# Performance work log

Hardware: AMD Instinct MI355X
Metric: run time of the kernel (lower is better)

Reference implementation:

```python
import jax, jax.numpy as jnp
import numpy as np

# Config matching init_kwargs
C, H_IMG, W_IMG = 3, 224, 224
N_PATCHES = 14
PS = H_IMG // N_PATCHES            # 16
INPUT_D = C * PS * PS              # 768
HID = 768
N_HEADS = 12
DH = HID // N_HEADS                # 64
N_BLOCKS = 12
MLP_RATIO = 4
SEQ = N_PATCHES * N_PATCHES + 1    # 197
EPS = 1e-5


def _pos_embed():
    # sin on even dims, cos on odd dims, exponent uses (j - j%2)/d  (faithful to loop)
    i = jnp.arange(SEQ, dtype=jnp.float32)[:, None]
    j = jnp.arange(HID, dtype=jnp.float32)[None, :]
    expo = (j - jnp.mod(j, 2.0)) / HID
    ang = i / jnp.power(10000.0, expo)
    return jnp.where(jnp.mod(jnp.arange(HID), 2) == 0, jnp.sin(ang), jnp.cos(ang))


def setup_inputs() -> dict:
    key = jax.random.key(0)
    ks = jax.random.split(key, 16)
    s = 0.02
    d_ff = MLP_RATIO * HID
    inp = {
        'images': jax.random.normal(ks[0], (16, C, H_IMG, W_IMG), dtype=jnp.float32),
        'w_map': jax.random.normal(ks[1], (HID, INPUT_D), dtype=jnp.float32) * s,
        'b_map': jnp.zeros((HID,), dtype=jnp.float32),
        'class_token': jax.random.uniform(ks[2], (1, HID), dtype=jnp.float32),
        'pos_embed': _pos_embed(),
        'qw': jax.random.normal(ks[3], (N_BLOCKS, N_HEADS, DH, DH), dtype=jnp.float32) * s,
        'qb': jnp.zeros((N_BLOCKS, N_HEADS, DH), dtype=jnp.float32),
        'kw': jax.random.normal(ks[4], (N_BLOCKS, N_HEADS, DH, DH), dtype=jnp.float32) * s,
        'kb': jnp.zeros((N_BLOCKS, N_HEADS, DH), dtype=jnp.float32),
        'vw': jax.random.normal(ks[5], (N_BLOCKS, N_HEADS, DH, DH), dtype=jnp.float32) * s,
        'vb': jnp.zeros((N_BLOCKS, N_HEADS, DH), dtype=jnp.float32),
        'ln1_w': jnp.ones((N_BLOCKS, HID), dtype=jnp.float32),
        'ln1_b': jnp.zeros((N_BLOCKS, HID), dtype=jnp.float32),
        'ln2_w': jnp.ones((N_BLOCKS, HID), dtype=jnp.float32),
        'ln2_b': jnp.zeros((N_BLOCKS, HID), dtype=jnp.float32),
        'mlp_w1': jax.random.normal(ks[6], (N_BLOCKS, d_ff, HID), dtype=jnp.float32) * s,
        'mlp_b1': jnp.zeros((N_BLOCKS, d_ff), dtype=jnp.float32),
        'mlp_w2': jax.random.normal(ks[7], (N_BLOCKS, HID, d_ff), dtype=jnp.float32) * s,
        'mlp_b2': jnp.zeros((N_BLOCKS, HID), dtype=jnp.float32),
    }
    return inp


def _layernorm(x, w, b):
    mu = jnp.mean(x, axis=-1, keepdims=True)
    var = jnp.mean(jnp.square(x - mu), axis=-1, keepdims=True)
    return (x - mu) * jax.lax.rsqrt(var + EPS) * w + b


def _patchify(images):
    # [N,C,H,W] -> [N, np^2, C*ps*ps]; per-patch flatten order is (c, ph, pw)
    n = images.shape[0]
    x = images.reshape(n, C, N_PATCHES, PS, N_PATCHES, PS)
    x = x.transpose(0, 2, 4, 1, 3, 5)  # n, pi, pj, c, ph, pw
    return x.reshape(n, N_PATCHES * N_PATCHES, INPUT_D)


def _msa(x, qw, qb, kw, kb, vw, vb):
    # x: [B,S,D]; per-head Linear on head slices; torch Linear: y = x @ W.T + b
    b_, s_, _ = x.shape
    xh = x.reshape(b_, s_, N_HEADS, DH)
    q = jnp.einsum('bshd,hod->bsho', xh, qw) + qb
    k = jnp.einsum('bshd,hod->bsho', xh, kw) + kb
    v = jnp.einsum('bshd,hod->bsho', xh, vw) + vb
    attn = jax.nn.softmax(jnp.einsum('bsho,btho->bhst', q, k) / (DH ** 0.5), axis=-1)
    out = jnp.einsum('bhst,btho->bsho', attn, v)
    return out.reshape(b_, s_, HID)


def reference(images, w_map, b_map, class_token, pos_embed, qw, qb, kw, kb, vw, vb,
              ln1_w, ln1_b, ln2_w, ln2_b, mlp_w1, mlp_b1, mlp_w2, mlp_b2):
    patches = _patchify(images)                       # [N, 196, 768]
    tokens = patches @ w_map.T + b_map                # [N, 196, HID]
    n = tokens.shape[0]
    cls = jnp.broadcast_to(class_token[None], (n, 1, HID))
    out = jnp.concatenate([cls, tokens], axis=1) + pos_embed[None]  # [N, SEQ, HID]
    for l in range(N_BLOCKS):
        out = out + _msa(_layernorm(out, ln1_w[l], ln1_b[l]),
                         qw[l], qb[l], kw[l], kb[l], vw[l], vb[l])
        h = _layernorm(out, ln2_w[l], ln2_b[l])
        h = jax.nn.gelu(h @ mlp_w1[l].T + mlp_b1[l], approximate=False)
        out = out + (h @ mlp_w2[l].T + mlp_b2[l])
    return out
```

## Files before the change

### kernel.cpp

```cpp
#include <hip/hip_runtime.h>
#include <hip/hip_bf16.h>
#include <math.h>

typedef __attribute__((ext_vector_type(4))) float f32x4;
typedef __attribute__((ext_vector_type(8))) __bf16 bf16x8;
typedef __attribute__((ext_vector_type(8))) short short8;
typedef __attribute__((ext_vector_type(4))) unsigned short us4;
typedef __attribute__((ext_vector_type(8))) unsigned short us8;

#define B_    16
#define SEQ_  197
#define TOK_  3152
#define HID_  768
#define MPAD_ 3200
#define NP_   3136
#define DFF_  3072
#define PSZ_  (MPAD_ * HID_)
#define QKVP_ 14336
#define BHN_  192

__device__ __forceinline__ unsigned short f2bf(float x) {
  union { float f; unsigned int u; } v; v.f = x;
  unsigned int r = v.u + 0x7fffu + ((v.u >> 16) & 1u);
  return (unsigned short)(r >> 16);
}

__device__ __forceinline__ float bf2f(unsigned short u) {
  union { unsigned int i; float f; } v; v.i = ((unsigned int)u) << 16; return v.f;
}

__device__ __forceinline__ f32x4 mfma16(bf16x8 a, bf16x8 b, f32x4 c) {
  return __builtin_amdgcn_mfma_f32_16x16x32_bf16(a, b, c, 0, 0, 0);
}

__device__ __forceinline__ void cp16(const void* g, void* l) {
  __builtin_amdgcn_global_load_lds((__attribute__((address_space(1))) void*)(g),
                                   (__attribute__((address_space(3))) void*)(l),
                                   16, 0, 0);
}

__device__ __forceinline__ float gelu_f(float x) {
  float y = x * (1.5957691216f + 0.0713548162f * x * x);
  float e = __expf(y);
  float r = 1.0f / (1.0f + e);
  return x - x * r;
}

__device__ __forceinline__ void conv8(const float* __restrict__ s, unsigned short* __restrict__ d, int c) {
  const float* sp = s + (size_t)c * 8;
  f32x4 v0 = *(const f32x4*)sp;
  f32x4 v1 = *(const f32x4*)(sp + 4);
  us8 o;
  o[0] = f2bf(v0[0]); o[1] = f2bf(v0[1]); o[2] = f2bf(v0[2]); o[3] = f2bf(v0[3]);
  o[4] = f2bf(v1[0]); o[5] = f2bf(v1[1]); o[6] = f2bf(v1[2]); o[7] = f2bf(v1[3]);
  *(us8*)(d + (size_t)c * 8) = o;
}

__global__ __launch_bounds__(256) void patchcls_kernel(const float* __restrict__ img,
                                                       unsigned short* __restrict__ Pb,
                                                       const float* __restrict__ ct,
                                                       const float* __restrict__ pos,
                                                       float* __restrict__ X,
                                                       const float* __restrict__ wmap,
                                                       unsigned short* __restrict__ Wmb,
                                                       const float* __restrict__ cw1,
                                                       unsigned short* __restrict__ cd1,
                                                       const float* __restrict__ cw2,
                                                       unsigned short* __restrict__ cd2) {
  int bid = blockIdx.x;
  if (bid >= 2736) {
    int bb = bid - 2736;
    const float* s; unsigned short* d;
    if (bb < 1152) { s = cw1; d = cd1; } else { s = cw2; d = cd2; bb -= 1152; }
    conv8(s, d, bb * 256 + threadIdx.x);
    return;
  }
  if (bid >= 2448) {
    int c = (bid - 2448) * 256 + threadIdx.x;
    conv8(wmap, Wmb, c);
    return;
  }
  if (bid >= 2400) {
    int j = (bid - 2400) * 256 + threadIdx.x;
    if (j < B_ * HID_) {
      int b = j / HID_, t = j - b * HID_;
      X[(size_t)b * SEQ_ * HID_ + t] = ct[t] + pos[t];
    }
    return;
  }
  int gid = bid * 256 + threadIdx.x;
  int m = gid / 192;
  int j4 = (gid - m * 192) * 4;
  us4 o;
  if (m < NP_) {
    int n = m / 196, p = m - n * 196;
    int pi = p / 14, pj = p - pi * 14;
    int c = j4 >> 8, rem = j4 & 255, ph = rem >> 4, pw = rem & 15;
    const float* src = img + (((size_t)(n * 3 + c) * 224 + pi * 16 + ph) * 224 + pj * 16 + pw);
    f32x4 v = *(const f32x4*)src;
    o[0] = f2bf(v[0]); o[1] = f2bf(v[1]); o[2] = f2bf(v[2]); o[3] = f2bf(v[3]);
  } else {
    o[0] = 0; o[1] = 0; o[2] = 0; o[3] = 0;
  }
  *(us4*)(Pb + (size_t)m * HID_ + j4) = o;
}

__global__ __launch_bounds__(256) void convw_kernel(const float* __restrict__ s1, unsigned short* __restrict__ d1,
                                                    const float* __restrict__ s2, unsigned short* __restrict__ d2,
                                                    int nchunks) {
  int half = gridDim.x >> 1;
  int b = blockIdx.x;
  const float* s; unsigned short* d;
  if (b < half) { s = s1; d = d1; } else { s = s2; d = d2; b -= half; }
  int c = b * 256 + threadIdx.x;
  if (c >= nchunks) return;
  conv8(s, d, c);
}

__global__ __launch_bounds__(256) void gemm_embed(const unsigned short* __restrict__ A,
                                                  const unsigned short* __restrict__ Bw,
                                                  const float* __restrict__ bias,
                                                  const float* __restrict__ pos,
                                                  float* __restrict__ Xout) {
  constexpr int MI = 2, NJ = 2, BM = 64, BN = 64;
  __shared__ unsigned short As[BM * 64];
  __shared__ unsigned short Bs[BN * 64];
  const int tid = threadIdx.x;
  const int w = tid >> 6, lane = tid & 63;
  const int lr = lane & 15, kg = lane >> 4;
  int bid = blockIdx.x;
  int cpx = gridDim.x >> 3;
  int swz = (bid & 7) * cpx + (bid >> 3);
  const int by = swz / 12, bx = swz - by * 12;
  const int m0 = by * BM, n0 = bx * BN;
  const int wr = w >> 1, wc = w & 1;
  const f32x4 z4 = {0.f, 0.f, 0.f, 0.f};
  f32x4 acc[MI][NJ];
#pragma unroll
  for (int i = 0; i < MI; ++i)
#pragma unroll
    for (int j = 0; j < NJ; ++j) acc[i][j] = z4;
  for (int k0 = 0; k0 < 768; k0 += 64) {
#pragma unroll
    for (int is = 0; is < MI; ++is) {
      int chunk = is * 256 + tid;
      int row = chunk >> 3, cc = (chunk & 7) * 8;
      cp16(A + (size_t)(m0 + row) * 768 + k0 + cc, As + is * 2048 + w * 512);
    }
#pragma unroll
    for (int is = 0; is < NJ; ++is) {
      int chunk = is * 256 + tid;
      int row = chunk >> 3, cc = (chunk & 7) * 8;
      cp16(Bw + (size_t)(n0 + row) * 768 + k0 + cc, Bs + is * 2048 + w * 512);
    }
    __syncthreads();
#pragma unroll
    for (int kk = 0; kk < 64; kk += 32) {
      bf16x8 af[MI], bfr[NJ];
#pragma unroll
      for (int i = 0; i < MI; ++i)
        af[i] = *(const bf16x8*)&As[(wr * (BM / 2) + i * 16 + lr) * 64 + kk + kg * 8];
#pragma unroll
      for (int j = 0; j < NJ; ++j)
        bfr[j] = *(const bf16x8*)&Bs[(wc * (BN / 2) + j * 16 + lr) * 64 + kk + kg * 8];
#pragma unroll
      for (int i = 0; i < MI; ++i)
#pragma unroll
        for (int j = 0; j < NJ; ++j)
          acc[i][j] = mfma16(af[i], bfr[j], acc[i][j]);
    }
    __syncthreads();
  }
#pragma unroll
  for (int i = 0; i < MI; ++i) {
    int mbase = m0 + wr * (BM / 2) + i * 16 + kg * 4;
#pragma unroll
    for (int j = 0; j < NJ; ++j) {
      int col = n0 + wc * (BN / 2) + j * 16 + lr;
#pragma unroll
      for (int qr = 0; qr < 4; ++qr) {
        int m = mbase + qr;
        if (m < NP_) {
          int nimg = m / 196;
          int tok = m + nimg + 1;
          int prow = m - nimg * 196 + 1;
          Xout[(size_t)tok * HID_ + col] = acc[i][j][qr] + bias[col] + pos[(size_t)prow * HID_ + col];
        }
      }
    }
  }
}

template<int EPI, int NT>
__global__ __launch_bounds__(512, 2) void gemm4b(const unsigned short* __restrict__ A,
                                                 const unsigned short* __restrict__ Bw,
                                                 int ldk, int gx, int gy,
                                                 const float* __restrict__ bias,
                                                 unsigned short* __restrict__ Pout,
                                                 unsigned short* __restrict__ Hout) {
  __shared__ unsigned short lds4[32768];
  const int tid = threadIdx.x;
  const int wid = tid >> 6, lane = tid & 63;
  const int lr = lane & 15, kg = lane >> 4;
  const int wm = wid >> 2, wn = wid & 3;
  const int nwg = gridDim.x;
  const int q = nwg >> 3, r = nwg & 7;
  const int xcd = blockIdx.x & 7, idx = blockIdx.x >> 3;
  const int wgid = (xcd < r ? xcd * (q + 1) : r * (q + 1) + (xcd - r) * q) + idx;
  const int bx = wgid % gx;
  const int rest = wgid / gx;
  const int by = rest % gy;
  const int z = rest / gy;
  const int m0 = by * 128, n0 = bx * 128;
  const unsigned short* Abase = A + (size_t)m0 * ldk + z * (NT * 32);
  const unsigned short* Bbase = Bw + (size_t)n0 * ldk + z * (NT * 32);

  const int ra = tid >> 2, ka = (tid & 3) * 8;
  const int wbase = wid * 512;

#pragma unroll
  for (int t = 0; t < 3; ++t) {
    unsigned short* lb = lds4 + t * 8192;
    cp16(Abase + (size_t)ra * ldk + ka + t * 32, lb + wbase);
    cp16(Bbase + (size_t)ra * ldk + ka + t * 32, lb + 4096 + wbase);
  }

  const f32x4 z4 = {0.f, 0.f, 0.f, 0.f};
  f32x4 acc[4][2];
#pragma unroll
  for (int i = 0; i < 4; ++i)
#pragma unroll
    for (int j = 0; j < 2; ++j) acc[i][j] = z4;

#pragma unroll 1
  for (int k = 0; k < NT; ++k) {
    asm volatile("s_waitcnt vmcnt(4)" ::: "memory");
    __builtin_amdgcn_s_barrier();
    __builtin_amdgcn_sched_barrier(0);
    const unsigned short* lp = lds4 + (k & 3) * 8192;
    const int tn = k + 3;
    const int ts = (tn >= NT) ? tn - NT : tn;
    unsigned short* tb = lds4 + (tn & 3) * 8192;
    bf16x8 af[4], bfr[2];
#pragma unroll
    for (int i = 0; i < 4; ++i)
      af[i] = *(const bf16x8*)(lp + (wm * 64 + i * 16 + lr) * 32 + kg * 8);
#pragma unroll
    for (int j = 0; j < 2; ++j)
      bfr[j] = *(const bf16x8*)(lp + 4096 + (wn * 32 + j * 16 + lr) * 32 + kg * 8);
    cp16(Abase + (size_t)ra * ldk + ka + ts * 32, tb + wbase);
    cp16(Bbase + (size_t)ra * ldk + ka + ts * 32, tb + 4096 + wbase);
    __builtin_amdgcn_s_barrier();
    __builtin_amdgcn_s_setprio(1);
#pragma unroll
    for (int i = 0; i < 4; ++i)
#pragma unroll
      for (int j = 0; j < 2; ++j) acc[i][j] = mfma16(af[i], bfr[j], acc[i][j]);
    __builtin_amdgcn_s_setprio(0);
  }

#pragma unroll
  for (int i = 0; i < 4; ++i) {
    int mbase = m0 + wm * 64 + i * 16 + kg * 4;
#pragma unroll
    for (int j = 0; j < 2; ++j) {
      int col = n0 + wn * 32 + j * 16 + lr;
      float bv = (EPI == 1) ? bias[col] : 0.f;
#pragma unroll
      for (int qr = 0; qr < 4; ++qr) {
        int m = mbase + qr;
        if (m < TOK_) {
          float v = acc[i][j][qr];
          if (EPI == 1) {
            Hout[(size_t)m * 3072 + col] = f2bf(gelu_f(v + bv));
          } else {
            Pout[(size_t)z * PSZ_ + (size_t)m * 768 + col] = f2bf(v);
          }
        }
      }
    }
  }
}

template<int MODE>
__global__ __launch_bounds__(256) void ln_kernel(float* __restrict__ X,
                                                 const unsigned short* __restrict__ P, const float* __restrict__ pb,
                                                 const float* __restrict__ gw, const float* __restrict__ gb,
                                                 unsigned short* __restrict__ Y,
                                                 const float* __restrict__ cw1, unsigned short* __restrict__ cd1,
                                                 const float* __restrict__ cw2, unsigned short* __restrict__ cd2) {
  int bb = (int)blockIdx.x - 800;
  if (bb >= 0) {
    const float* s; unsigned short* d;
    if (bb < 1152) { s = cw1; d = cd1; } else { s = cw2; d = cd2; bb -= 1152; }
    conv8(s, d, bb * 256 + threadIdx.x);
    return;
  }
  int row = blockIdx.x * 4 + (threadIdx.x >> 6);
  int lane = threadIdx.x & 63;
  if (row >= MPAD_) return;
  size_t base = (size_t)row * HID_;
  if (row >= TOK_) {
    us4 zz; zz[0] = 0; zz[1] = 0; zz[2] = 0; zz[3] = 0;
#pragma unroll
    for (int i = 0; i < 3; ++i) *(us4*)(Y + base + i * 256 + lane * 4) = zz;
    return;
  }
  f32x4 xv[3];
  float s1 = 0.f, s2 = 0.f;
#pragma unroll
  for (int i = 0; i < 3; ++i) {
    int cb = i * 256 + lane * 4;
    f32x4 v = *(const f32x4*)(X + base + cb);
    if (MODE == 2) {
      const unsigned short* pp = P + base + cb;
      us4 p0 = *(const us4*)(pp);
      us4 p1 = *(const us4*)(pp + PSZ_);
      f32x4 bb2 = *(const f32x4*)(pb + cb);
#pragma unroll
      for (int e = 0; e < 4; ++e)
        v[e] += bf2f(p0[e]) + bf2f(p1[e]) + bb2[e];
      *(f32x4*)(X + base + cb) = v;
    }
    xv[i] = v;
    s1 += v[0] + v[1] + v[2] + v[3];
    s2 += v[0] * v[0] + v[1] * v[1] + v[2] * v[2] + v[3] * v[3];
  }
#pragma unroll
  for (int d = 1; d < 64; d <<= 1) {
    s1 += __shfl_xor(s1, d);
    s2 += __shfl_xor(s2, d);
  }
  float mu = s1 * (1.f / 768.f);
  float var = s2 * (1.f / 768.f) - mu * mu;
  float rs = rsqrtf(var + 1e-5f);
#pragma unroll
  for (int i = 0; i < 3; ++i) {
    int cb = i * 256 + lane * 4;
    us4 o;
#pragma unroll
    for (int e = 0; e < 4; ++e)
      o[e] = f2bf((xv[i][e] - mu) * rs * gw[cb + e] + gb[cb + e]);
    *(us4*)(Y + base + cb) = o;
  }
}

__global__ __launch_bounds__(256) void redfin_kernel(float* __restrict__ X, const unsigned short* __restrict__ P,
                                                     const float* __restrict__ b2) {
  int i = blockIdx.x * 256 + threadIdx.x;
  if (i >= TOK_ * 192) return;
  int m = i / 192, c4 = (i - m * 192) * 4;
  size_t off = (size_t)m * HID_ + c4;
  f32x4 v = *(const f32x4*)(X + off);
  const unsigned short* pp = P + off;
  us4 p0 = *(const us4*)(pp);
  us4 p1 = *(const us4*)(pp + PSZ_);
  f32x4 bb = *(const f32x4*)(b2 + c4);
#pragma unroll
  for (int e = 0; e < 4; ++e)
    v[e] += bf2f(p0[e]) + bf2f(p1[e]) + bb[e];
  *(f32x4*)(X + off) = v;
}

__device__ __forceinline__ void loadw_frags(const float* __restrict__ W, int lr, int kg, bf16x8* wf) {
#pragma unroll
  for (int j = 0; j < 4; ++j)
#pragma unroll
    for (int kk = 0; kk < 2; ++kk) {
      const float* wp = W + (j * 16 + lr) * 64 + kk * 32 + kg * 8;
      f32x4 w0 = *(const f32x4*)wp;
      f32x4 w1 = *(const f32x4*)(wp + 4);
      short8 t;
      t[0] = (short)f2bf(w0[0]); t[1] = (short)f2bf(w0[1]); t[2] = (short)f2bf(w0[2]); t[3] = (short)f2bf(w0[3]);
      t[4] = (short)f2bf(w1[0]); t[5] = (short)f2bf(w1[1]); t[6] = (short)f2bf(w1[2]); t[7] = (short)f2bf(w1[3]);
      wf[j * 2 + kk] = __builtin_bit_cast(bf16x8, t);
    }
}

__global__ __launch_bounds__(128) void qkvproj_kernel(const unsigned short* __restrict__ Y,
                                                      const float* __restrict__ qw, const float* __restrict__ qb,
                                                      const float* __restrict__ kw, const float* __restrict__ kb,
                                                      const float* __restrict__ vw, const float* __restrict__ vb,
                                                      unsigned short* __restrict__ Qo,
                                                      unsigned short* __restrict__ Ko,
                                                      unsigned short* __restrict__ Vto) {
  const int blk = blockIdx.x;
  const int half = blk & 1;
  const int bp = blk >> 1;
  const int p = bp % 3, bh = bp / 3;
  const int b = bh / 12, h = bh - b * 12;
  const int wv = threadIdx.x >> 6, lane = threadIdx.x & 63;
  const int lr = lane & 15, kg = lane >> 4;
  const int ws = half * 2 + wv;
  const float* W; const float* bs; unsigned short* out;
  if (p == 0)      { W = qw + h * 4096; bs = qb + h * 64; out = Qo; }
  else if (p == 1) { W = kw + h * 4096; bs = kb + h * 64; out = Ko; }
  else             { W = vw + h * 4096; bs = vb + h * 64; out = Vto; }
  const float scale = (p == 0) ? 0.125f : 1.0f;
  bf16x8 wf[8];
  loadw_frags(W, lr, kg, wf);
  float bj[4];
#pragma unroll
  for (int j = 0; j < 4; ++j) bj[j] = bs[j * 16 + lr];
  out += (size_t)bh * QKVP_;
  const f32x4 z4 = {0.f, 0.f, 0.f, 0.f};
  const short8 zs = {0, 0, 0, 0, 0, 0, 0, 0};
#pragma unroll
  for (int i = 0; i < 4; ++i) {
    int t = ws + 4 * i;
    if (t < 14) {
      int s = t * 16 + lr;
      bf16x8 a0 = __builtin_bit_cast(bf16x8, zs), a1 = a0;
      if (s < SEQ_) {
        const unsigned short* yp = Y + (size_t)(b * SEQ_ + s) * HID_ + h * 64 + kg * 8;
        a0 = *(const bf16x8*)yp;
        a1 = *(const bf16x8*)(yp + 32);
      }
      f32x4 acc[4] = {z4, z4, z4, z4};
#pragma unroll
      for (int j = 0; j < 4; ++j) {
        acc[j] = mfma16(a0, wf[j * 2 + 0], acc[j]);
        acc[j] = mfma16(a1, wf[j * 2 + 1], acc[j]);
      }
      if (p == 2) {
#pragma unroll
        for (int j = 0; j < 4; ++j) {
          us4 pk;
#pragma unroll
          for (int qr = 0; qr < 4; ++qr) {
            int srow = t * 16 + kg * 4 + qr;
            pk[qr] = (srow < SEQ_) ? f2bf(acc[j][qr] + bj[j]) : (unsigned short)0;
          }
          *(us4*)&out[(j * 16 + lr) * 224 + t * 16 + kg * 4] = pk;
        }
      } else {
#pragma unroll
        for (int j = 0; j < 4; ++j)
#pragma unroll
          for (int qr = 0; qr < 4; ++qr) {
            int row = t * 16 + kg * 4 + qr;
            out[row * 64 + j * 16 + lr] = f2bf((acc[j][qr] + bj[j]) * scale);
          }
      }
    }
  }
}

__global__ __launch_bounds__(64) void attn_kernel(const unsigned short* __restrict__ Qb,
                                                  const unsigned short* __restrict__ Kb,
                                                  const unsigned short* __restrict__ Vtb,
                                                  float* __restrict__ X) {
  __shared__ unsigned short plds[16 * 232];
  const int blk = blockIdx.x;
  const int qt = blk % 13, bh = blk / 13;
  const int b = bh / 12, h = bh - b * 12;
  const int lane = threadIdx.x;
  const int lr = lane & 15, kg = lane >> 4;
  const f32x4 z4 = {0.f, 0.f, 0.f, 0.f};
  const unsigned short* Qp = Qb + (size_t)bh * QKVP_;
  const unsigned short* Kp = Kb + (size_t)bh * QKVP_;
  const unsigned short* Vp = Vtb + (size_t)bh * QKVP_;
  {
    int rr = lane >> 2, c0 = 208 + (lane & 3) * 4;
    us4 zz; zz[0] = 0; zz[1] = 0; zz[2] = 0; zz[3] = 0;
    *(us4*)&plds[rr * 232 + c0] = zz;
  }
  bf16x8 aq0 = *(const bf16x8*)&Qp[(qt * 16 + lr) * 64 + kg * 8];
  bf16x8 aq1 = *(const bf16x8*)&Qp[(qt * 16 + lr) * 64 + 32 + kg * 8];
  f32x4 s[13];
#pragma unroll
  for (int nt = 0; nt < 13; ++nt) {
    const unsigned short* kp = Kp + (nt * 16 + lr) * 64 + kg * 8;
    bf16x8 b0 = *(const bf16x8*)kp;
    bf16x8 b1 = *(const bf16x8*)(kp + 32);
    f32x4 acc = mfma16(aq0, b0, z4);
    s[nt] = mfma16(aq1, b1, acc);
  }
#pragma unroll
  for (int qr = 0; qr < 4; ++qr) {
    float mx = -1e30f;
#pragma unroll
    for (int nt = 0; nt < 13; ++nt) {
      float v = (nt == 12 && lr >= 5) ? -1e30f : s[nt][qr];
      mx = fmaxf(mx, v);
    }
    mx = fmaxf(mx, __shfl_xor(mx, 1));
    mx = fmaxf(mx, __shfl_xor(mx, 2));
    mx = fmaxf(mx, __shfl_xor(mx, 4));
    mx = fmaxf(mx, __shfl_xor(mx, 8));
    float sum = 0.f;
#pragma unroll
    for (int nt = 0; nt < 13; ++nt) {
      float e = (nt == 12 && lr >= 5) ? 0.f : __expf(s[nt][qr] - mx);
      s[nt][qr] = e;
      sum += e;
    }
    sum += __shfl_xor(sum, 1);
    sum += __shfl_xor(sum, 2);
    sum += __shfl_xor(sum, 4);
    sum += __shfl_xor(sum, 8);
    float inv = 1.f / sum;
#pragma unroll
    for (int nt = 0; nt < 13; ++nt)
      plds[(kg * 4 + qr) * 232 + nt * 16 + lr] = f2bf(s[nt][qr] * inv);
  }
  asm volatile("s_waitcnt lgkmcnt(0)" ::: "memory");
  __builtin_amdgcn_sched_barrier(0);
  f32x4 ao[4] = {z4, z4, z4, z4};
#pragma unroll
  for (int kt = 0; kt < 7; ++kt) {
    bf16x8 pa = *(const bf16x8*)&plds[lr * 232 + kt * 32 + kg * 8];
#pragma unroll
    for (int j = 0; j < 4; ++j) {
      bf16x8 bv = *(const bf16x8*)&Vp[(j * 16 + lr) * 224 + kt * 32 + kg * 8];
      ao[j] = mfma16(pa, bv, ao[j]);
    }
  }
#pragma unroll
  for (int j = 0; j < 4; ++j)
#pragma unroll
    for (int qr = 0; qr < 4; ++qr) {
      int ss = qt * 16 + kg * 4 + qr;
      if (ss < SEQ_) {
        size_t xi = (size_t)(b * SEQ_ + ss) * HID_ + h * 64 + j * 16 + lr;
        X[xi] += ao[j][qr];
      }
    }
}

extern "C" void kernel_launch(void* const* d_in, const int* in_sizes, int n_in,
                              void* d_out, int out_size, void* d_ws, size_t ws_size,
                              hipStream_t stream) {
  const float* images = (const float*)d_in[0];
  const float* w_map  = (const float*)d_in[1];
  const float* b_map  = (const float*)d_in[2];
  const float* ctok   = (const float*)d_in[3];
  const float* pos    = (const float*)d_in[4];
  const float* qw   = (const float*)d_in[5];
  const float* qb   = (const float*)d_in[6];
  const float* kw   = (const float*)d_in[7];
  const float* kb   = (const float*)d_in[8];
  const float* vw   = (const float*)d_in[9];
  const float* vb   = (const float*)d_in[10];
  const float* ln1w = (const float*)d_in[11];
  const float* ln1b = (const float*)d_in[12];
  const float* ln2w = (const float*)d_in[13];
  const float* ln2b = (const float*)d_in[14];
  const float* w1   = (const float*)d_in[15];
  const float* b1   = (const float*)d_in[16];
  const float* w2   = (const float*)d_in[17];
  const float* b2   = (const float*)d_in[18];

  float* X = (float*)d_out;

  unsigned short* Y    = (unsigned short*)d_ws;
  unsigned short* Wmb  = Y + (size_t)MPAD_ * HID_;
  unsigned short* Hb   = Wmb + (size_t)768 * 768;
  unsigned short* Pp   = Hb + (size_t)MPAD_ * DFF_;
  unsigned short* Wr   = Pp + 2 * (size_t)PSZ_;

  unsigned short* Qb  = Hb;
  unsigned short* Kb2 = Hb + (size_t)BHN_ * QKVP_;
  unsigned short* Vtb = Hb + 2 * (size_t)BHN_ * QKVP_;

  const size_t L1 = (size_t)DFF_ * HID_;
  const size_t need = ((size_t)MPAD_ * HID_ + (size_t)768 * 768 + (size_t)MPAD_ * DFF_ +
                       2 * (size_t)PSZ_ + 24 * L1) * 2;
  const bool big = ws_size >= need;
  unsigned short* W1r = Wr;
  unsigned short* W2r = Wr + (big ? 12 * L1 : L1);

  patchcls_kernel<<<big ? 5040 : 2736, 256, 0, stream>>>(images, Y, ctok, pos, X,
                                                         w_map, Wmb, w1, W1r, w2, W2r);
  gemm_embed<<<600, 256, 0, stream>>>(Y, Wmb, b_map, pos, X);

  for (int l = 0; l < 12; ++l) {
    unsigned short* W1p = big ? W1r + l * L1 : W1r;
    unsigned short* W2p = big ? W2r + l * L1 : W2r;
    if (l == 0)
      ln_kernel<0><<<800, 256, 0, stream>>>(X, nullptr, nullptr,
                                            ln1w + l * 768, ln1b + l * 768, Y,
                                            nullptr, nullptr, nullptr, nullptr);
    else
      ln_kernel<2><<<800, 256, 0, stream>>>(X, Pp, b2 + (l - 1) * 768,
                                            ln1w + l * 768, ln1b + l * 768, Y,
                                            nullptr, nullptr, nullptr, nullptr);
    qkvproj_kernel<<<1152, 128, 0, stream>>>(Y,
                                             qw + (size_t)l * 49152, qb + l * 768,
                                             kw + (size_t)l * 49152, kb + l * 768,
                                             vw + (size_t)l * 49152, vb + l * 768,
                                             Qb, Kb2, Vtb);
    attn_kernel<<<2496, 64, 0, stream>>>(Qb, Kb2, Vtb, X);
    const bool cvt = big && (l < 11);
    ln_kernel<0><<<cvt ? 3104 : 800, 256, 0, stream>>>(X, nullptr, nullptr,
                                                       ln2w + l * 768, ln2b + l * 768, Y,
                                                       cvt ? w1 + (size_t)(l + 1) * L1 : nullptr,
                                                       cvt ? W1r + (size_t)(l + 1) * L1 : nullptr,
                                                       cvt ? w2 + (size_t)(l + 1) * L1 : nullptr,
                                                       cvt ? W2r + (size_t)(l + 1) * L1 : nullptr);
    if (!big)
      convw_kernel<<<2304, 256, 0, stream>>>(w1 + (size_t)l * L1, W1p,
                                             w2 + (size_t)l * L1, W2p, 294912);
    gemm4b<1, 24><<<600, 512, 0, stream>>>(Y, W1p, 768, 24, 25, b1 + l * 3072, nullptr, Hb);
    gemm4b<3, 48><<<300, 512, 0, stream>>>(Hb, W2p, 3072, 6, 25, nullptr, Pp, nullptr);
  }
  redfin_kernel<<<2364, 256, 0, stream>>>(X, Pp, b2 + 11 * 768);
}
```

Measured before the change: 1.433 ms.

## Use 4-wave 64x64 warp tiles and XOR-swizzled LDS in MLP GEMM

Moves the MLP GEMM kernel from 8 waves per block to 4 waves, giving each wave a 64x64 output tile (4x4 MFMAs) instead of 64x32. This raises register-level reuse of the A and B fragments loaded from LDS. It also adds an XOR swizzle on the k-chunk offset for both the global-to-LDS copies and the fragment reads, to cut LDS bank conflicts. Each thread now issues twice as many async copies, so the vmcnt wait threshold rises from 4 to 8. Doubling the accumulators raises register pressure, and halving the waves per block may reduce latency hiding.

New measurement: 1.574 ms. +9.8%, slower.

```diff
diff --git a/kernel.cpp b/kernel.cpp
--- a/kernel.cpp
+++ b/kernel.cpp
@@ -192,7 +192,7 @@
 }
 
 template<int EPI, int NT>
-__global__ __launch_bounds__(512, 2) void gemm4b(const unsigned short* __restrict__ A,
+__global__ __launch_bounds__(256, 2) void gemm4b(const unsigned short* __restrict__ A,
                                                  const unsigned short* __restrict__ Bw,
                                                  int ldk, int gx, int gy,
                                                  const float* __restrict__ bias,
@@ -202,7 +202,7 @@
   const int tid = threadIdx.x;
   const int wid = tid >> 6, lane = tid & 63;
   const int lr = lane & 15, kg = lane >> 4;
-  const int wm = wid >> 2, wn = wid & 3;
+  const int wm = wid >> 1, wn = wid & 1;
   const int nwg = gridDim.x;
   const int q = nwg >> 3, r = nwg & 7;
   const int xcd = blockIdx.x & 7, idx = blockIdx.x >> 3;
@@ -215,47 +215,64 @@
   const unsigned short* Abase = A + (size_t)m0 * ldk + z * (NT * 32);
   const unsigned short* Bbase = Bw + (size_t)n0 * ldk + z * (NT * 32);
 
-  const int ra = tid >> 2, ka = (tid & 3) * 8;
-  const int wbase = wid * 512;
+  const int r0 = tid >> 2, u0 = tid & 3;
+  const int r1 = 64 + r0;
+  const int sk0 = ((u0 ^ ((r0 >> 1) & 3)) * 8);
+  const int sk1 = ((u0 ^ ((r1 >> 1) & 3)) * 8);
+  const int d0 = wid * 512;
+  const int d1 = 2048 + wid * 512;
 
 #pragma unroll
   for (int t = 0; t < 3; ++t) {
     unsigned short* lb = lds4 + t * 8192;
-    cp16(Abase + (size_t)ra * ldk + ka + t * 32, lb + wbase);
-    cp16(Bbase + (size_t)ra * ldk + ka + t * 32, lb + 4096 + wbase);
+    cp16(Abase + (size_t)r0 * ldk + sk0 + t * 32, lb + d0);
+    cp16(Abase + (size_t)r1 * ldk + sk1 + t * 32, lb + d1);
+    cp16(Bbase + (size_t)r0 * ldk + sk0 + t * 32, lb + 4096 + d0);
+    cp16(Bbase + (size_t)r1 * ldk + sk1 + t * 32, lb + 4096 + d1);
+  }
+
+  int offA[4], offB[4];
+#pragma unroll
+  for (int i = 0; i < 4; ++i) {
+    int ra_ = wm * 64 + i * 16 + lr;
+    offA[i] = ra_ * 32 + ((kg ^ ((ra_ >> 1) & 3)) * 8);
+    int rb_ = wn * 64 + i * 16 + lr;
+    offB[i] = rb_ * 32 + ((kg ^ ((rb_ >> 1) & 3)) * 8);
   }
 
   const f32x4 z4 = {0.f, 0.f, 0.f, 0.f};
-  f32x4 acc[4][2];
+  f32x4 acc[4][4];
 #pragma unroll
   for (int i = 0; i < 4; ++i)
 #pragma unroll
-    for (int j = 0; j < 2; ++j) acc[i][j] = z4;
+    for (int j = 0; j < 4; ++j) acc[i][j] = z4;
 
 #pragma unroll 1
   for (int k = 0; k < NT; ++k) {
-    asm volatile("s_waitcnt vmcnt(4)" ::: "memory");
+    asm volatile("s_waitcnt vmcnt(8)" ::: "memory");
     __builtin_amdgcn_s_barrier();
     __builtin_amdgcn_sched_barrier(0);
     const unsigned short* lp = lds4 + (k & 3) * 8192;
     const int tn = k + 3;
     const int ts = (tn >= NT) ? tn - NT : tn;
     unsigned short* tb = lds4 + (tn & 3) * 8192;
-    bf16x8 af[4], bfr[2];
+    bf16x8 af[4], bfr[4];
 #pragma unroll
     for (int i = 0; i < 4; ++i)
-      af[i] = *(const bf16x8*)(lp + (wm * 64 + i * 16 + lr) * 32 + kg * 8);
-#pragma unroll
-    for (int j = 0; j < 2; ++j)
-      bfr[j] = *(const bf16x8*)(lp + 4096 + (wn * 32 + j * 16 + lr) * 32 + kg * 8);
-    cp16(Abase + (size_t)ra * ldk + ka + ts * 32, tb + wbase);
-    cp16(Bbase + (size_t)ra * ldk + ka + ts * 32, tb + 4096 + wbase);
+      af[i] = *(const bf16x8*)(lp + offA[i]);
+#pragma unroll
+    for (int j = 0; j < 4; ++j)
+      bfr[j] = *(const bf16x8*)(lp + 4096 + offB[j]);
+    cp16(Abase + (size_t)r0 * ldk + sk0 + ts * 32, tb + d0);
+    cp16(Abase + (size_t)r1 * ldk + sk1 + ts * 32, tb + d1);
+    cp16(Bbase + (size_t)r0 * ldk + sk0 + ts * 32, tb + 4096 + d0);
+    cp16(Bbase + (size_t)r1 * ldk + sk1 + ts * 32, tb + 4096 + d1);
     __builtin_amdgcn_s_barrier();
     __builtin_amdgcn_s_setprio(1);
 #pragma unroll
     for (int i = 0; i < 4; ++i)
 #pragma unroll
-      for (int j = 0; j < 2; ++j) acc[i][j] = mfma16(af[i], bfr[j], acc[i][j]);
+      for (int j = 0; j < 4; ++j) acc[i][j] = mfma16(af[i], bfr[j], acc[i][j]);
     __builtin_amdgcn_s_setprio(0);
   }
 
@@ -263,8 +280,8 @@
   for (int i = 0; i < 4; ++i) {
     int mbase = m0 + wm * 64 + i * 16 + kg * 4;
 #pragma unroll
-    for (int j = 0; j < 2; ++j) {
-      int col = n0 + wn * 32 + j * 16 + lr;
+    for (int j = 0; j < 4; ++j) {
+      int col = n0 + wn * 64 + j * 16 + lr;
       float bv = (EPI == 1) ? bias[col] : 0.f;
 #pragma unroll
       for (int qr = 0; qr < 4; ++qr) {
@@ -601,8 +618,8 @@
     if (!big)
       convw_kernel<<<2304, 256, 0, stream>>>(w1 + (size_t)l * L1, W1p,
                                              w2 + (size_t)l * L1, W2p, 294912);
-    gemm4b<1, 24><<<600, 512, 0, stream>>>(Y, W1p, 768, 24, 25, b1 + l * 3072, nullptr, Hb);
-    gemm4b<3, 48><<<300, 512, 0, stream>>>(Hb, W2p, 3072, 6, 25, nullptr, Pp, nullptr);
+    gemm4b<1, 24><<<600, 256, 0, stream>>>(Y, W1p, 768, 24, 25, b1 + l * 3072, nullptr, Hb);
+    gemm4b<3, 48><<<300, 256, 0, stream>>>(Hb, W2p, 3072, 6, 25, nullptr, Pp, nullptr);
   }
   redfin_kernel<<<2364, 256, 0, stream>>>(X, Pp, b2 + 11 * 768);
 }
```

## Swizzle GEMM LDS layout and split MLP down-projection into four K slices

Applied to the files above, without the earlier changes.

The GEMM now XOR-swizzles the 8-element K chunk position by row in LDS, on both the async copy side and the fragment read side, to avoid LDS bank conflicts. The second MLP GEMM is split-K with four partial slices instead of two (NT 24, 600 workgroups). This raises occupancy on the 300-workgroup launch. The LayerNorm and final reduction kernels now sum four bf16 partials, and the workspace grows to hold them. The cost is extra partial-sum memory traffic and more bf16 rounding of the partials.

Result: no change. 1.429 ms (-0.3%).

```diff
diff --git a/kernel.cpp b/kernel.cpp
--- a/kernel.cpp
+++ b/kernel.cpp
@@ -215,14 +215,27 @@
   const unsigned short* Abase = A + (size_t)m0 * ldk + z * (NT * 32);
   const unsigned short* Bbase = Bw + (size_t)n0 * ldk + z * (NT * 32);
 
-  const int ra = tid >> 2, ka = (tid & 3) * 8;
+  const int ra = tid >> 2, ua = tid & 3;
+  const int sk = (ua ^ ((ra >> 1) & 3)) * 8;
   const int wbase = wid * 512;
 
 #pragma unroll
   for (int t = 0; t < 3; ++t) {
     unsigned short* lb = lds4 + t * 8192;
-    cp16(Abase + (size_t)ra * ldk + ka + t * 32, lb + wbase);
-    cp16(Bbase + (size_t)ra * ldk + ka + t * 32, lb + 4096 + wbase);
+    cp16(Abase + (size_t)ra * ldk + sk + t * 32, lb + wbase);
+    cp16(Bbase + (size_t)ra * ldk + sk + t * 32, lb + 4096 + wbase);
+  }
+
+  int offA[4], offB[2];
+#pragma unroll
+  for (int i = 0; i < 4; ++i) {
+    int rr = wm * 64 + i * 16 + lr;
+    offA[i] = rr * 32 + ((kg ^ ((rr >> 1) & 3)) * 8);
+  }
+#pragma unroll
+  for (int j = 0; j < 2; ++j) {
+    int rr = wn * 32 + j * 16 + lr;
+    offB[j] = rr * 32 + ((kg ^ ((rr >> 1) & 3)) * 8);
   }
 
   const f32x4 z4 = {0.f, 0.f, 0.f, 0.f};
@@ -244,12 +257,12 @@
     bf16x8 af[4], bfr[2];
 #pragma unroll
     for (int i = 0; i < 4; ++i)
-      af[i] = *(const bf16x8*)(lp + (wm * 64 + i * 16 + lr) * 32 + kg * 8);
+      af[i] = *(const bf16x8*)(lp + offA[i]);
 #pragma unroll
     for (int j = 0; j < 2; ++j)
-      bfr[j] = *(const bf16x8*)(lp + 4096 + (wn * 32 + j * 16 + lr) * 32 + kg * 8);
-    cp16(Abase + (size_t)ra * ldk + ka + ts * 32, tb + wbase);
-    cp16(Bbase + (size_t)ra * ldk + ka + ts * 32, tb + 4096 + wbase);
+      bfr[j] = *(const bf16x8*)(lp + 4096 + offB[j]);
+    cp16(Abase + (size_t)ra * ldk + sk + ts * 32, tb + wbase);
+    cp16(Bbase + (size_t)ra * ldk + sk + ts * 32, tb + 4096 + wbase);
     __builtin_amdgcn_s_barrier();
     __builtin_amdgcn_s_setprio(1);
 #pragma unroll
@@ -316,10 +329,12 @@
       const unsigned short* pp = P + base + cb;
       us4 p0 = *(const us4*)(pp);
       us4 p1 = *(const us4*)(pp + PSZ_);
+      us4 p2 = *(const us4*)(pp + 2 * (size_t)PSZ_);
+      us4 p3 = *(const us4*)(pp + 3 * (size_t)PSZ_);
       f32x4 bb2 = *(const f32x4*)(pb + cb);
 #pragma unroll
       for (int e = 0; e < 4; ++e)
-        v[e] += bf2f(p0[e]) + bf2f(p1[e]) + bb2[e];
+        v[e] += bf2f(p0[e]) + bf2f(p1[e]) + bf2f(p2[e]) + bf2f(p3[e]) + bb2[e];
       *(f32x4*)(X + base + cb) = v;
     }
     xv[i] = v;
@@ -355,10 +370,12 @@
   const unsigned short* pp = P + off;
   us4 p0 = *(const us4*)(pp);
   us4 p1 = *(const us4*)(pp + PSZ_);
+  us4 p2 = *(const us4*)(pp + 2 * (size_t)PSZ_);
+  us4 p3 = *(const us4*)(pp + 3 * (size_t)PSZ_);
   f32x4 bb = *(const f32x4*)(b2 + c4);
 #pragma unroll
   for (int e = 0; e < 4; ++e)
-    v[e] += bf2f(p0[e]) + bf2f(p1[e]) + bb[e];
+    v[e] += bf2f(p0[e]) + bf2f(p1[e]) + bf2f(p2[e]) + bf2f(p3[e]) + bb[e];
   *(f32x4*)(X + off) = v;
 }
 
@@ -557,7 +574,7 @@
   unsigned short* Wmb  = Y + (size_t)MPAD_ * HID_;
   unsigned short* Hb   = Wmb + (size_t)768 * 768;
   unsigned short* Pp   = Hb + (size_t)MPAD_ * DFF_;
-  unsigned short* Wr   = Pp + 2 * (size_t)PSZ_;
+  unsigned short* Wr   = Pp + 4 * (size_t)PSZ_;
 
   unsigned short* Qb  = Hb;
   unsigned short* Kb2 = Hb + (size_t)BHN_ * QKVP_;
@@ -565,7 +582,7 @@
 
   const size_t L1 = (size_t)DFF_ * HID_;
   const size_t need = ((size_t)MPAD_ * HID_ + (size_t)768 * 768 + (size_t)MPAD_ * DFF_ +
-                       2 * (size_t)PSZ_ + 24 * L1) * 2;
+                       4 * (size_t)PSZ_ + 24 * L1) * 2;
   const bool big = ws_size >= need;
   unsigned short* W1r = Wr;
   unsigned short* W2r = Wr + (big ? 12 * L1 : L1);
@@ -602,7 +619,7 @@
       convw_kernel<<<2304, 256, 0, stream>>>(w1 + (size_t)l * L1, W1p,
                                              w2 + (size_t)l * L1, W2p, 294912);
     gemm4b<1, 24><<<600, 512, 0, stream>>>(Y, W1p, 768, 24, 25, b1 + l * 3072, nullptr, Hb);
-    gemm4b<3, 48><<<300, 512, 0, stream>>>(Hb, W2p, 3072, 6, 25, nullptr, Pp, nullptr);
+    gemm4b<3, 24><<<600, 512, 0, stream>>>(Hb, W2p, 3072, 6, 25, nullptr, Pp, nullptr);
   }
   redfin_kernel<<<2364, 256, 0, stream>>>(X, Pp, b2 + 11 * 768);
 }
```
